# Kernel optimization log

Measured on AMD Instinct MI355X. Metric: run time of the kernel, lower is better.

Reference implementation:

```python
import jax, jax.numpy as jnp
import numpy as np

B, N, DIM = 8, 4096, 512
H, DH = 8, 64
INNER = H * DH
MIN_FREQ = 1.0 / 64
SCALE = 1.0
ROT_DIM = DH // 2  # 32, per spatial axis
EPS = 1e-5


def setup_inputs() -> dict:
    key = jax.random.key(0)
    ks = jax.random.split(key, 6)
    x = jax.random.normal(ks[0], (B, N, DIM), dtype=jnp.float32)
    pos = jax.random.uniform(ks[1], (B, N, 2), dtype=jnp.float32)
    W_qkv = jax.random.normal(ks[2], (3 * INNER, DIM), dtype=jnp.float32) * (1.0 / DH)
    gamma_k = jnp.ones((DH,), jnp.float32)
    beta_k = jnp.zeros((DH,), jnp.float32)
    gamma_v = jnp.ones((DH,), jnp.float32)
    beta_v = jnp.zeros((DH,), jnp.float32)
    W_out = jax.random.normal(ks[3], (DIM, INNER), dtype=jnp.float32) * (1.0 / np.sqrt(INNER))
    b_out = jnp.zeros((DIM,), jnp.float32)
    return {"x": x, "pos": pos, "W_qkv": W_qkv, "gamma_k": gamma_k, "beta_k": beta_k,
            "gamma_v": gamma_v, "beta_v": beta_v, "W_out": W_out, "b_out": b_out}


def _layernorm(t, gamma, beta):
    mu = jnp.mean(t, axis=-1, keepdims=True)
    var = jnp.var(t, axis=-1, keepdims=True)
    return (t - mu) * jax.lax.rsqrt(var + EPS) * gamma + beta


def _rotate_half(t):
    # '... (j d) -> ... j d' with j=2, then cat(-x2, x1)
    d = t.shape[-1] // 2
    x1, x2 = t[..., :d], t[..., d:]
    return jnp.concatenate((-x2, x1), axis=-1)


def _apply_rot(t, freqs):
    return t * jnp.cos(freqs) + _rotate_half(t) * jnp.sin(freqs)


def _freqs(coord):
    # coord: [b, n]; inv_freq over rotary half-dim
    inv_freq = 1.0 / (10000.0 ** (jnp.arange(0, ROT_DIM, 2, dtype=jnp.float32) / ROT_DIM))
    t = coord * (SCALE / MIN_FREQ)
    f = t[..., None] * inv_freq  # [b, n, ROT_DIM//2]
    return jnp.concatenate((f, f), axis=-1)[:, None, :, :]  # [b, 1, n, ROT_DIM]


def reference(x, pos, W_qkv, gamma_k, beta_k, gamma_v, beta_v, W_out, b_out):
    b, n, _ = x.shape
    qkv = x @ W_qkv.T  # [b, n, 3*INNER]
    q, k, v = jnp.split(qkv, 3, axis=-1)
    split = lambda t: t.reshape(b, n, H, DH).transpose(0, 2, 1, 3)  # b h n d
    q, k, v = split(q), split(k), split(v)

    # Galerkin: LayerNorm on K and V over head dim
    k = _layernorm(k, gamma_k, beta_k)
    v = _layernorm(v, gamma_v, beta_v)

    # 2D rotary on q, k: first half of head dim uses x-coords, second half y-coords
    fx, fy = _freqs(pos[..., 0]), _freqs(pos[..., 1])
    rot2d = lambda t: jnp.concatenate(
        (_apply_rot(t[..., :ROT_DIM], fx), _apply_rot(t[..., ROT_DIM:], fy)), axis=-1)
    q = rot2d(q)
    k = rot2d(k)

    # Associative linear attention: (K^T V) then Q @ (.) / n
    dots = jnp.einsum('bhnd,bhne->bhde', k, v)  # [b, h, d, d]
    out = jnp.einsum('bhnd,bhde->bhne', q, dots) * (1.0 / n)
    out = out.transpose(0, 2, 1, 3).reshape(b, n, INNER)
    return out @ W_out.T + b_out
```

## Files before the change

kernel.cpp:

```cpp
#include <hip/hip_runtime.h>
#include <math.h>

#define NB 8
#define NN 4096
#define NDIM 512
#define NH 8
#define NDH 64
#define QKVC 1536
#define NROWS (NB * NN)
#define EPSF 1e-5f
#define INV_N (1.0f / 4096.0f)
#define L2_10K_16 0.8304820237218406f

typedef __bf16 bf16x8_t __attribute__((ext_vector_type(8)));
typedef float f32x4_t __attribute__((ext_vector_type(4)));
typedef unsigned short u16x8 __attribute__((ext_vector_type(8)));

__device__ inline unsigned short f2bf(float f) {
    unsigned u = __builtin_bit_cast(unsigned, f);
    u += 0x7fff + ((u >> 16) & 1);
    return (unsigned short)(u >> 16);
}
__device__ inline float bf2f(unsigned short u) {
    unsigned v = (unsigned)u << 16;
    return __builtin_bit_cast(float, v);
}

#define GLOAD_LDS16(g, s) __builtin_amdgcn_global_load_lds(                    \
    (const __attribute__((address_space(1))) void*)(g),                        \
    (__attribute__((address_space(3))) void*)(s), 16, 0, 0)

#define VMCNT3 asm volatile("s_waitcnt vmcnt(3)" ::: "memory")
#define VMCNT0 asm volatile("s_waitcnt vmcnt(0)" ::: "memory")
#define BARF   { __builtin_amdgcn_s_barrier(); asm volatile("" ::: "memory"); }

__device__ inline void cvt8v(const float* __restrict__ s,
                             unsigned short* __restrict__ d, int i)
{
    float4 a = *(const float4*)(s + i);
    float4 b = *(const float4*)(s + i + 4);
    ushort4 lo, hi;
    lo.x = f2bf(a.x); lo.y = f2bf(a.y); lo.z = f2bf(a.z); lo.w = f2bf(a.w);
    hi.x = f2bf(b.x); hi.y = f2bf(b.y); hi.z = f2bf(b.z); hi.w = f2bf(b.w);
    *(ushort4*)(d + i)     = lo;
    *(ushort4*)(d + i + 4) = hi;
}

__global__ __launch_bounds__(256)
void cvt_all(const float* __restrict__ x,  const float* __restrict__ wq,
             const float* __restrict__ wo,
             unsigned short* __restrict__ xb, unsigned short* __restrict__ wqb,
             unsigned short* __restrict__ wob, float* __restrict__ dots)
{
    const int bid = blockIdx.x, t = threadIdx.x;
    if (bid < 8192) {
        cvt8v(x, xb, (bid * 256 + t) * 8);
    } else if (bid < 8576) {
        cvt8v(wq, wqb, ((bid - 8192) * 256 + t) * 8);
    } else if (bid < 8704) {
        cvt8v(wo, wob, ((bid - 8576) * 256 + t) * 8);
    } else {
        const float4 z = {0.f, 0.f, 0.f, 0.f};
        float4* dp = (float4*)dots + (size_t)((bid - 8704) * 256 + t) * 4;
        dp[0] = z; dp[1] = z; dp[2] = z; dp[3] = z;
    }
}

__global__ __launch_bounds__(512, 4)
void gemm_kv_fused(const unsigned short* __restrict__ A,
                   const unsigned short* __restrict__ Bm,
                   const float* __restrict__ pos,
                   const float* __restrict__ gk, const float* __restrict__ bk,
                   const float* __restrict__ gv, const float* __restrict__ bvv,
                   unsigned short* __restrict__ kT,
                   unsigned short* __restrict__ vT)
{
    __shared__ __align__(16) unsigned short lds[24576];

    const int tid  = threadIdx.x;
    const int wave = tid >> 6;
    const int lane = tid & 63;

    int flat = blockIdx.y * 8 + blockIdx.x;
    flat = (flat & 7) * 128 + (flat >> 3);
    const int bx = flat & 7;
    const int by = flat >> 3;
    const int m0 = by * 256;
    const int n0 = bx * 128;

    const int warp_m = wave >> 1;
    const int warp_n = wave & 1;
    const int fr = lane & 15;
    const int fq = lane >> 4;
    const int ch0 = ((fq ^ ((fr >> 1) & 3)) << 3);

    const int rl = tid >> 2;
    const int cs = (((tid & 3) ^ ((rl >> 1) & 3)) << 3);
    const unsigned short* Asrc = A  + (size_t)(m0 + rl) * NDIM + cs;
    const unsigned short* Bsrc = Bm + (size_t)(n0 + rl) * NDIM + cs;
    const int sdst = wave * 512;

#define STG_A(tt, c) GLOAD_LDS16(Asrc + (size_t)((c) * 128) * NDIM + (tt) * 32, \
        &lds[(((tt) & 1) * 8192) + ((c) * 4096) + sdst])
#define STG_B(tt)    GLOAD_LDS16(Bsrc + (tt) * 32, \
        &lds[16384 + (((tt) & 1) * 4096) + sdst])

    f32x4_t acc[4][4] = {};

    STG_A(0, 0); STG_A(0, 1); STG_B(0);

    #pragma unroll 2
    for (int tt = 0; tt < 16; ++tt) {
        BARF;
        if (tt < 15) { STG_A(tt + 1, 0); STG_A(tt + 1, 1); STG_B(tt + 1); VMCNT3; }
        else VMCNT0;
        BARF;
        bf16x8_t af[4], bfr[4];
        const int ab = (tt & 1) * 8192;
        const int bb = 16384 + (tt & 1) * 4096;
        #pragma unroll
        for (int mi = 0; mi < 4; ++mi)
            af[mi] = *(const bf16x8_t*)&lds[ab + (warp_m * 64 + mi * 16 + fr) * 32 + ch0];
        #pragma unroll
        for (int nj = 0; nj < 4; ++nj)
            bfr[nj] = *(const bf16x8_t*)&lds[bb + (warp_n * 64 + nj * 16 + fr) * 32 + ch0];
        __builtin_amdgcn_s_setprio(1);
        #pragma unroll
        for (int mi = 0; mi < 4; ++mi)
            #pragma unroll
            for (int nj = 0; nj < 4; ++nj)
                acc[mi][nj] = __builtin_amdgcn_mfma_f32_16x16x32_bf16(
                    af[mi], bfr[nj], acc[mi][nj], 0, 0, 0);
        __builtin_amdgcn_s_setprio(0);
    }
#undef STG_A
#undef STG_B

    const int nc = n0 + warp_n * 64;
    const int isK = (nc < 512);
    const int c  = lane & 15;
    const int g4 = (lane >> 4) * 4;
    const int mrow0 = m0 + warp_m * 64;
    const int h = (nc >> 6) & 7;

    {
        const float* gamma = isK ? gk : gv;
        const float* beta  = isK ? bk : bvv;
        float gm[4], bt[4];
        #pragma unroll
        for (int j = 0; j < 4; ++j) { gm[j] = gamma[j * 16 + c]; bt[j] = beta[j * 16 + c]; }
        #pragma unroll
        for (int i = 0; i < 4; ++i)
            #pragma unroll
            for (int r = 0; r < 4; ++r) {
                float t0 = acc[i][0][r], t1 = acc[i][1][r];
                float t2 = acc[i][2][r], t3 = acc[i][3][r];
                float s  = t0 + t1 + t2 + t3;
                float ss = t0*t0 + t1*t1 + t2*t2 + t3*t3;
                #pragma unroll
                for (int msk = 1; msk < 16; msk <<= 1) {
                    s  += __shfl_xor(s,  msk, 64);
                    ss += __shfl_xor(ss, msk, 64);
                }
                const float mu = s * (1.0f / 64.0f);
                const float rs = rsqrtf(ss * (1.0f / 64.0f) - mu * mu + EPSF);
                acc[i][0][r] = (t0 - mu) * rs * gm[0] + bt[0];
                acc[i][1][r] = (t1 - mu) * rs * gm[1] + bt[1];
                acc[i][2][r] = (t2 - mu) * rs * gm[2] + bt[2];
                acc[i][3][r] = (t3 - mu) * rs * gm[3] + bt[3];
            }
    }
    if (isK) {
        const float Kc = 64.0f * exp2f(-(float)c * L2_10K_16);
        #pragma unroll
        for (int i = 0; i < 4; ++i)
            #pragma unroll
            for (int r = 0; r < 4; ++r) {
                const int row = mrow0 + i * 16 + g4 + r;
                const float2 p = ((const float2*)pos)[row];
                float sx, cx, sy, cy;
                __sincosf(p.x * Kc, &sx, &cx);
                __sincosf(p.y * Kc, &sy, &cy);
                const float t0 = acc[i][0][r], t1 = acc[i][1][r];
                const float t2 = acc[i][2][r], t3 = acc[i][3][r];
                acc[i][0][r] = t0 * cx - t1 * sx;
                acc[i][1][r] = t1 * cx + t0 * sx;
                acc[i][2][r] = t2 * cy - t3 * sy;
                acc[i][3][r] = t3 * cy + t2 * sy;
            }
    }
    unsigned short* T = isK ? kT : vT;
    #pragma unroll
    for (int i = 0; i < 4; ++i) {
        const int row = mrow0 + i * 16 + g4;
        const int bb = row >> 12;
        const int nl = row & 4095;
        #pragma unroll
        for (int j = 0; j < 4; ++j) {
            ushort4 o;
            o.x = f2bf(acc[i][j][0]); o.y = f2bf(acc[i][j][1]);
            o.z = f2bf(acc[i][j][2]); o.w = f2bf(acc[i][j][3]);
            *(ushort4*)(T + ((size_t)((bb * NH + h) * 64 + j * 16 + c)) * NN + nl) = o;
        }
    }
}

__global__ __launch_bounds__(512, 4)
void gemm_q_fused(const unsigned short* __restrict__ A,
                  const unsigned short* __restrict__ Bm,
                  const float* __restrict__ pos,
                  unsigned short* __restrict__ qb)
{
    __shared__ __align__(16) unsigned short lds[24576];

    const int tid  = threadIdx.x;
    const int wave = tid >> 6;
    const int lane = tid & 63;

    int flat = blockIdx.y * 4 + blockIdx.x;
    flat = (flat & 7) * 64 + (flat >> 3);
    const int bx = flat & 3;
    const int by = flat >> 2;
    const int m0 = by * 256;
    const int n0 = bx * 128;

    const int warp_m = wave >> 1;
    const int warp_n = wave & 1;
    const int fr = lane & 15;
    const int fq = lane >> 4;
    const int ch0 = ((fq ^ ((fr >> 1) & 3)) << 3);

    const int rl = tid >> 2;
    const int cs = (((tid & 3) ^ ((rl >> 1) & 3)) << 3);
    const unsigned short* Asrc = A  + (size_t)(m0 + rl) * NDIM + cs;
    const unsigned short* Bsrc = Bm + (size_t)(n0 + rl) * NDIM + cs;
    const int sdst = wave * 512;

#define STG_A(tt, c) GLOAD_LDS16(Asrc + (size_t)((c) * 128) * NDIM + (tt) * 32, \
        &lds[(((tt) & 1) * 8192) + ((c) * 4096) + sdst])
#define STG_B(tt)    GLOAD_LDS16(Bsrc + (tt) * 32, \
        &lds[16384 + (((tt) & 1) * 4096) + sdst])

    f32x4_t acc[4][4] = {};

    STG_A(0, 0); STG_A(0, 1); STG_B(0);

    #pragma unroll 2
    for (int tt = 0; tt < 16; ++tt) {
        BARF;
        if (tt < 15) { STG_A(tt + 1, 0); STG_A(tt + 1, 1); STG_B(tt + 1); VMCNT3; }
        else VMCNT0;
        BARF;
        bf16x8_t af[4], bfr[4];
        const int ab = (tt & 1) * 8192;
        const int bb = 16384 + (tt & 1) * 4096;
        #pragma unroll
        for (int mi = 0; mi < 4; ++mi)
            af[mi] = *(const bf16x8_t*)&lds[ab + (warp_m * 64 + mi * 16 + fr) * 32 + ch0];
        #pragma unroll
        for (int nj = 0; nj < 4; ++nj)
            bfr[nj] = *(const bf16x8_t*)&lds[bb + (warp_n * 64 + nj * 16 + fr) * 32 + ch0];
        __builtin_amdgcn_s_setprio(1);
        #pragma unroll
        for (int mi = 0; mi < 4; ++mi)
            #pragma unroll
            for (int nj = 0; nj < 4; ++nj)
                acc[mi][nj] = __builtin_amdgcn_mfma_f32_16x16x32_bf16(
                    af[mi], bfr[nj], acc[mi][nj], 0, 0, 0);
        __builtin_amdgcn_s_setprio(0);
    }
#undef STG_A
#undef STG_B

    const int nc = n0 + warp_n * 64;
    const int c  = lane & 15;
    const int g4 = (lane >> 4) * 4;
    const int mrow0 = m0 + warp_m * 64;

    {
        const float Kc = 64.0f * exp2f(-(float)c * L2_10K_16);
        #pragma unroll
        for (int i = 0; i < 4; ++i)
            #pragma unroll
            for (int r = 0; r < 4; ++r) {
                const int row = mrow0 + i * 16 + g4 + r;
                const float2 p = ((const float2*)pos)[row];
                float sx, cx, sy, cy;
                __sincosf(p.x * Kc, &sx, &cx);
                __sincosf(p.y * Kc, &sy, &cy);
                const float t0 = acc[i][0][r], t1 = acc[i][1][r];
                const float t2 = acc[i][2][r], t3 = acc[i][3][r];
                acc[i][0][r] = t0 * cx - t1 * sx;
                acc[i][1][r] = t1 * cx + t0 * sx;
                acc[i][2][r] = t2 * cy - t3 * sy;
                acc[i][3][r] = t3 * cy + t2 * sy;
            }
    }
    #pragma unroll
    for (int i = 0; i < 4; ++i)
        #pragma unroll
        for (int j = 0; j < 4; ++j) {
            unsigned short* qp = qb + (size_t)(mrow0 + i * 16 + g4) * NDIM
                               + nc + j * 16 + c;
            #pragma unroll
            for (int r = 0; r < 4; ++r)
                qp[(size_t)r * NDIM] = f2bf(acc[i][j][r]);
        }
}

__global__ __launch_bounds__(256)
void dots_mfma(const unsigned short* __restrict__ kT,
               const unsigned short* __restrict__ vT,
               float* __restrict__ dots)
{
    __shared__ __align__(16) unsigned short sk[2][64 * 64];
    __shared__ __align__(16) unsigned short sv[2][64 * 64];
    const int t = threadIdx.x;
    const int w = t >> 6, l = t & 63;
    const int bh = blockIdx.z * NH + blockIdx.y;
    const int n0 = blockIdx.x * 512;

    const int r8 = l >> 3;
    const int cs = ((l & 7) ^ r8) * 8;
    const unsigned short* ksrc = kT + (size_t)(bh * 64 + w * 16 + r8) * NN + n0 + cs;
    const unsigned short* vsrc = vT + (size_t)(bh * 64 + w * 16 + r8) * NN + n0 + cs;

#define STGK(buf, kt, q) GLOAD_LDS16(ksrc + (size_t)(q) * 8 * NN + (kt), \
        &sk[buf][w * 1024 + (q) * 512])
#define STGV(buf, kt, q) GLOAD_LDS16(vsrc + (size_t)(q) * 8 * NN + (kt), \
        &sv[buf][w * 1024 + (q) * 512])

    const int fr = l & 15, fq = l >> 4;
    const int doff = (w >> 1) * 32, eoff = (w & 1) * 32;

    f32x4_t acc[2][2] = {};

    STGK(0, 0, 0); STGK(0, 0, 1); STGV(0, 0, 0); STGV(0, 0, 1);

    for (int s = 0; s < 8; ++s) {
        const int buf = s & 1;
        asm volatile("s_waitcnt vmcnt(0)" ::: "memory");
        __builtin_amdgcn_s_barrier();
        bf16x8_t ak[2][2], bv[2][2];
        #pragma unroll
        for (int di = 0; di < 2; ++di)
            #pragma unroll
            for (int ks = 0; ks < 2; ++ks)
                ak[di][ks] = *(const bf16x8_t*)
                    &sk[buf][(doff + di * 16 + fr) * 64 + (((ks * 4 + fq) ^ (fr & 7)) * 8)];
        #pragma unroll
        for (int ej = 0; ej < 2; ++ej)
            #pragma unroll
            for (int ks = 0; ks < 2; ++ks)
                bv[ej][ks] = *(const bf16x8_t*)
                    &sv[buf][(eoff + ej * 16 + fr) * 64 + (((ks * 4 + fq) ^ (fr & 7)) * 8)];
        if (s + 1 < 8) {
            const int nb = buf ^ 1, kt = (s + 1) * 64;
            STGK(nb, kt, 0); STGK(nb, kt, 1); STGV(nb, kt, 0); STGV(nb, kt, 1);
        }
        #pragma unroll
        for (int ks = 0; ks < 2; ++ks)
            #pragma unroll
            for (int di = 0; di < 2; ++di)
                #pragma unroll
                for (int ej = 0; ej < 2; ++ej)
                    acc[di][ej] = __builtin_amdgcn_mfma_f32_16x16x32_bf16(
                        ak[di][ks], bv[ej][ks], acc[di][ej], 0, 0, 0);
    }
#undef STGK
#undef STGV

    float* dp = dots + (size_t)bh * 64 * 64;
    const int cc = l & 15;
    const int rr = (l >> 4) * 4;
    #pragma unroll
    for (int di = 0; di < 2; ++di)
        #pragma unroll
        for (int ej = 0; ej < 2; ++ej)
            #pragma unroll
            for (int r = 0; r < 4; ++r)
                atomicAdd(dp + (doff + di * 16 + rr + r) * 64 + eoff + ej * 16 + cc,
                          acc[di][ej][r]);
}

__global__ __launch_bounds__(256)
void dotsw_mfma(const unsigned short* __restrict__ Woutb,
                const float* __restrict__ dots,
                unsigned short* __restrict__ M2b)
{
    __shared__ unsigned short As[128 * 64];
    __shared__ unsigned short Bs[64 * 64];
    const int t = threadIdx.x;
    const int wave = t >> 6;
    const int lane = t & 63;
    const int dp0 = blockIdx.x * 128;
    const int h = blockIdx.y, b = blockIdx.z;

    const int srow = lane >> 3;
    const int scol = (lane & 7) * 8;
    const unsigned short* Ag = Woutb + (size_t)(dp0 + wave * 32 + srow) * NDIM
                             + h * NDH + scol;
    #pragma unroll
    for (int i = 0; i < 4; ++i)
        GLOAD_LDS16(Ag + (size_t)i * 8 * NDIM, As + wave * 2048 + i * 512);

    {
        const float* Dg = dots + (size_t)(b * NH + h) * 4096;
        const int dr = t >> 2;
        const int dc = (t & 3) * 16;
        const float* dgp = Dg + dr * 64 + dc;
        float4 f0 = *(const float4*)(dgp);
        float4 f1 = *(const float4*)(dgp + 4);
        float4 f2 = *(const float4*)(dgp + 8);
        float4 f3 = *(const float4*)(dgp + 12);
        ushort4 o0, o1, o2, o3;
        o0.x = f2bf(f0.x * INV_N); o0.y = f2bf(f0.y * INV_N);
        o0.z = f2bf(f0.z * INV_N); o0.w = f2bf(f0.w * INV_N);
        o1.x = f2bf(f1.x * INV_N); o1.y = f2bf(f1.y * INV_N);
        o1.z = f2bf(f1.z * INV_N); o1.w = f2bf(f1.w * INV_N);
        o2.x = f2bf(f2.x * INV_N); o2.y = f2bf(f2.y * INV_N);
        o2.z = f2bf(f2.z * INV_N); o2.w = f2bf(f2.w * INV_N);
        o3.x = f2bf(f3.x * INV_N); o3.y = f2bf(f3.y * INV_N);
        o3.z = f2bf(f3.z * INV_N); o3.w = f2bf(f3.w * INV_N);
        *(ushort4*)&Bs[dr * 64 + dc]      = o0;
        *(ushort4*)&Bs[dr * 64 + dc + 4]  = o1;
        *(ushort4*)&Bs[dr * 64 + dc + 8]  = o2;
        *(ushort4*)&Bs[dr * 64 + dc + 12] = o3;
    }
    __syncthreads();

    const int wm = (wave >> 1) * 64;
    const int wn = (wave & 1) * 32;
    const int fr = lane & 15;
    const int fq = (lane >> 4) * 8;

    f32x4_t acc[4][2] = {};
    #pragma unroll
    for (int kk = 0; kk < 2; ++kk) {
        bf16x8_t af[4], bf[2];
        #pragma unroll
        for (int i = 0; i < 4; ++i)
            af[i] = *(const bf16x8_t*)&As[(wm + i * 16 + fr) * 64 + kk * 32 + fq];
        #pragma unroll
        for (int j = 0; j < 2; ++j)
            bf[j] = *(const bf16x8_t*)&Bs[(wn + j * 16 + fr) * 64 + kk * 32 + fq];
        #pragma unroll
        for (int i = 0; i < 4; ++i)
            #pragma unroll
            for (int j = 0; j < 2; ++j)
                acc[i][j] = __builtin_amdgcn_mfma_f32_16x16x32_bf16(
                    af[i], bf[j], acc[i][j], 0, 0, 0);
    }

    const int c  = lane & 15;
    const int g4 = (lane >> 4) * 4;
    #pragma unroll
    for (int i = 0; i < 4; ++i)
        #pragma unroll
        for (int j = 0; j < 2; ++j) {
            unsigned short* mp = M2b + ((size_t)(b * NDIM) + dp0 + wm + i * 16 + g4) * NDIM
                               + h * NDH + wn + j * 16 + c;
            #pragma unroll
            for (int r = 0; r < 4; ++r)
                mp[(size_t)r * NDIM] = f2bf(acc[i][j][r]);
        }
}

__global__ __launch_bounds__(512, 4)
void gemm_out_mfma(const unsigned short* __restrict__ qb,
                   const unsigned short* __restrict__ M2b,
                   const float* __restrict__ bias, float* __restrict__ C)
{
    __shared__ __align__(16) unsigned short lds[24576];

    const int tid  = threadIdx.x;
    const int wave = tid >> 6;
    const int lane = tid & 63;

    int flat = blockIdx.y * 4 + blockIdx.x;
    flat = (flat & 7) * 64 + (flat >> 3);
    const int bx = flat & 3;
    const int by = flat >> 2;
    const int m0 = by * 256;
    const int n0 = bx * 128;
    const int b  = m0 >> 12;

    const int warp_m = wave >> 1;
    const int warp_n = wave & 1;
    const int fr = lane & 15;
    const int fq = lane >> 4;
    const int ch0 = ((fq ^ ((fr >> 1) & 3)) << 3);

    const int rl = tid >> 2;
    const int cs = (((tid & 3) ^ ((rl >> 1) & 3)) << 3);
    const unsigned short* Asrc = qb + (size_t)(m0 + rl) * NDIM + cs;
    const unsigned short* Bsrc = M2b + (size_t)b * NDIM * NDIM
                               + (size_t)(n0 + rl) * NDIM + cs;
    const int sdst = wave * 512;

#define STG_A(tt, c) GLOAD_LDS16(Asrc + (size_t)((c) * 128) * NDIM + (tt) * 32, \
        &lds[(((tt) & 1) * 8192) + ((c) * 4096) + sdst])
#define STG_B(tt)    GLOAD_LDS16(Bsrc + (tt) * 32, \
        &lds[16384 + (((tt) & 1) * 4096) + sdst])

    f32x4_t acc[4][4] = {};

    STG_A(0, 0); STG_A(0, 1); STG_B(0);

    #pragma unroll 2
    for (int tt = 0; tt < 16; ++tt) {
        BARF;
        if (tt < 15) { STG_A(tt + 1, 0); STG_A(tt + 1, 1); STG_B(tt + 1); VMCNT3; }
        else VMCNT0;
        BARF;
        bf16x8_t af[4], bfr[4];
        const int ab = (tt & 1) * 8192;
        const int bb = 16384 + (tt & 1) * 4096;
        #pragma unroll
        for (int mi = 0; mi < 4; ++mi)
            af[mi] = *(const bf16x8_t*)&lds[ab + (warp_m * 64 + mi * 16 + fr) * 32 + ch0];
        #pragma unroll
        for (int nj = 0; nj < 4; ++nj)
            bfr[nj] = *(const bf16x8_t*)&lds[bb + (warp_n * 64 + nj * 16 + fr) * 32 + ch0];
        __builtin_amdgcn_s_setprio(1);
        #pragma unroll
        for (int mi = 0; mi < 4; ++mi)
            #pragma unroll
            for (int nj = 0; nj < 4; ++nj)
                acc[mi][nj] = __builtin_amdgcn_mfma_f32_16x16x32_bf16(
                    af[mi], bfr[nj], acc[mi][nj], 0, 0, 0);
        __builtin_amdgcn_s_setprio(0);
    }
#undef STG_A
#undef STG_B

    const int c  = lane & 15;
    const int g4 = (lane >> 4) * 4;
    const int mrow0 = m0 + warp_m * 64;
    const int ncol = n0 + warp_n * 64;

    #pragma unroll
    for (int j = 0; j < 4; ++j) {
        const int col = ncol + j * 16 + c;
        const float bb = bias[col];
        #pragma unroll
        for (int i = 0; i < 4; ++i) {
            float* cp = C + (size_t)(mrow0 + i * 16 + g4) * NDIM + col;
            #pragma unroll
            for (int r = 0; r < 4; ++r)
                cp[(size_t)r * NDIM] = acc[i][j][r] + bb;
        }
    }
}

extern "C" void kernel_launch(void* const* d_in, const int* in_sizes, int n_in,
                              void* d_out, int out_size, void* d_ws, size_t ws_size,
                              hipStream_t stream)
{
    const float* x    = (const float*)d_in[0];
    const float* pos  = (const float*)d_in[1];
    const float* Wqkv = (const float*)d_in[2];
    const float* gk   = (const float*)d_in[3];
    const float* bk   = (const float*)d_in[4];
    const float* gv   = (const float*)d_in[5];
    const float* bv   = (const float*)d_in[6];
    const float* Wout = (const float*)d_in[7];
    const float* bout = (const float*)d_in[8];
    float* out = (float*)d_out;

    float* dots = (float*)d_ws;
    unsigned short* M2b     = (unsigned short*)(dots + (size_t)NB * NH * 64 * 64);
    unsigned short* qb      = M2b + (size_t)NB * NDIM * NDIM;
    unsigned short* kT      = qb + (size_t)NROWS * NDIM;
    unsigned short* vT      = kT + (size_t)NB * NH * NDH * NN;
    unsigned short* xb      = vT + (size_t)NB * NH * NDH * NN;
    unsigned short* Wqkvb   = xb + (size_t)NROWS * NDIM;
    unsigned short* Woutb   = Wqkvb + (size_t)QKVC * NDIM;

    cvt_all<<<dim3(8768), dim3(256), 0, stream>>>(x, Wqkv, Wout, xb, Wqkvb, Woutb, dots);
    gemm_kv_fused<<<dim3(8, NROWS / 256), dim3(512), 0, stream>>>(
        xb, Wqkvb + (size_t)512 * NDIM, pos, gk, bk, gv, bv, kT, vT);
    gemm_q_fused<<<dim3(4, NROWS / 256), dim3(512), 0, stream>>>(
        xb, Wqkvb, pos, qb);
    dots_mfma<<<dim3(NN / 512, NH, NB), dim3(256), 0, stream>>>(kT, vT, dots);
    dotsw_mfma<<<dim3(NDIM / 128, NH, NB), dim3(256), 0, stream>>>(Woutb, dots, M2b);
    gemm_out_mfma<<<dim3(NDIM / 128, NROWS / 256), dim3(512), 0, stream>>>(
        qb, M2b, bout, out);
}
```

Measured before the change: 265.1 us.

## Triple-buffer LDS staging in GEMMs and dots kernel with one barrier per step

Replaces the double-buffered LDS pipeline in the three GEMM kernels (now sharing a GEMM_CORE macro) with a three-stage ring that prefetches two tiles ahead. This lets each iteration use a single barrier instead of two. The dots kernel gets the same three-stage, two-ahead prefetch with a partial vmcnt wait and raised MFMA priority. The cost is 50% more LDS per block (72KB for the GEMMs), which could reduce how many blocks fit on a CU.

```diff
diff --git a/kernel.cpp b/kernel.cpp
--- a/kernel.cpp
+++ b/kernel.cpp
@@ -30,6 +30,7 @@
     (const __attribute__((address_space(1))) void*)(g),                        \
     (__attribute__((address_space(3))) void*)(s), 16, 0, 0)
 
+#define VMCNT4 asm volatile("s_waitcnt vmcnt(4)" ::: "memory")
 #define VMCNT3 asm volatile("s_waitcnt vmcnt(3)" ::: "memory")
 #define VMCNT0 asm volatile("s_waitcnt vmcnt(0)" ::: "memory")
 #define BARF   { __builtin_amdgcn_s_barrier(); asm volatile("" ::: "memory"); }
@@ -66,6 +67,47 @@
     }
 }
 
+#define GEMM_CORE(Asrc_, Bsrc_)                                                \
+    f32x4_t acc[4][4] = {};                                                    \
+    const int fr = lane & 15;                                                  \
+    const int fq = lane >> 4;                                                  \
+    const int ch0 = ((fq ^ ((fr >> 1) & 3)) << 3);                             \
+    const int rl = tid >> 2;                                                   \
+    const int cs = (((tid & 3) ^ ((rl >> 1) & 3)) << 3);                       \
+    const unsigned short* Asrc = (Asrc_) + (size_t)rl * NDIM + cs;             \
+    const unsigned short* Bsrc = (Bsrc_) + (size_t)rl * NDIM + cs;             \
+    const int sdst = wave * 512;                                               \
+    STG_A(0, 0); STG_A(0, 1); STG_B(0);                                        \
+    STG_A(1, 0); STG_A(1, 1); STG_B(1);                                        \
+    _Pragma("unroll")                                                          \
+    for (int tt = 0; tt < 16; ++tt) {                                          \
+        if (tt == 15) VMCNT0; else VMCNT3;                                     \
+        BARF;                                                                  \
+        if (tt < 14) { STG_A(tt + 2, 0); STG_A(tt + 2, 1); STG_B(tt + 2); }    \
+        bf16x8_t af[4], bfr[4];                                                \
+        const int ab = (tt % 3) * 12288;                                       \
+        const int bb = ab + 8192;                                              \
+        _Pragma("unroll")                                                      \
+        for (int mi = 0; mi < 4; ++mi)                                         \
+            af[mi] = *(const bf16x8_t*)&lds[ab + (warp_m * 64 + mi * 16 + fr) * 32 + ch0]; \
+        _Pragma("unroll")                                                      \
+        for (int nj = 0; nj < 4; ++nj)                                         \
+            bfr[nj] = *(const bf16x8_t*)&lds[bb + (warp_n * 64 + nj * 16 + fr) * 32 + ch0]; \
+        __builtin_amdgcn_s_setprio(1);                                         \
+        _Pragma("unroll")                                                      \
+        for (int mi = 0; mi < 4; ++mi)                                         \
+            _Pragma("unroll")                                                  \
+            for (int nj = 0; nj < 4; ++nj)                                     \
+                acc[mi][nj] = __builtin_amdgcn_mfma_f32_16x16x32_bf16(         \
+                    af[mi], bfr[nj], acc[mi][nj], 0, 0, 0);                    \
+        __builtin_amdgcn_s_setprio(0);                                         \
+    }
+
+#define STG_A(tt, c) GLOAD_LDS16(Asrc + (size_t)((c) * 128) * NDIM + (tt) * 32, \
+        &lds[((tt) % 3) * 12288 + ((c) * 4096) + sdst])
+#define STG_B(tt)    GLOAD_LDS16(Bsrc + (tt) * 32, \
+        &lds[((tt) % 3) * 12288 + 8192 + sdst])
+
 __global__ __launch_bounds__(512, 4)
 void gemm_kv_fused(const unsigned short* __restrict__ A,
                    const unsigned short* __restrict__ Bm,
@@ -75,7 +117,7 @@
                    unsigned short* __restrict__ kT,
                    unsigned short* __restrict__ vT)
 {
-    __shared__ __align__(16) unsigned short lds[24576];
+    __shared__ __align__(16) unsigned short lds[36864];
 
     const int tid  = threadIdx.x;
     const int wave = tid >> 6;
@@ -90,51 +132,8 @@
 
     const int warp_m = wave >> 1;
     const int warp_n = wave & 1;
-    const int fr = lane & 15;
-    const int fq = lane >> 4;
-    const int ch0 = ((fq ^ ((fr >> 1) & 3)) << 3);
-
-    const int rl = tid >> 2;
-    const int cs = (((tid & 3) ^ ((rl >> 1) & 3)) << 3);
-    const unsigned short* Asrc = A  + (size_t)(m0 + rl) * NDIM + cs;
-    const unsigned short* Bsrc = Bm + (size_t)(n0 + rl) * NDIM + cs;
-    const int sdst = wave * 512;
-
-#define STG_A(tt, c) GLOAD_LDS16(Asrc + (size_t)((c) * 128) * NDIM + (tt) * 32, \
-        &lds[(((tt) & 1) * 8192) + ((c) * 4096) + sdst])
-#define STG_B(tt)    GLOAD_LDS16(Bsrc + (tt) * 32, \
-        &lds[16384 + (((tt) & 1) * 4096) + sdst])
-
-    f32x4_t acc[4][4] = {};
-
-    STG_A(0, 0); STG_A(0, 1); STG_B(0);
-
-    #pragma unroll 2
-    for (int tt = 0; tt < 16; ++tt) {
-        BARF;
-        if (tt < 15) { STG_A(tt + 1, 0); STG_A(tt + 1, 1); STG_B(tt + 1); VMCNT3; }
-        else VMCNT0;
-        BARF;
-        bf16x8_t af[4], bfr[4];
-        const int ab = (tt & 1) * 8192;
-        const int bb = 16384 + (tt & 1) * 4096;
-        #pragma unroll
-        for (int mi = 0; mi < 4; ++mi)
-            af[mi] = *(const bf16x8_t*)&lds[ab + (warp_m * 64 + mi * 16 + fr) * 32 + ch0];
-        #pragma unroll
-        for (int nj = 0; nj < 4; ++nj)
-            bfr[nj] = *(const bf16x8_t*)&lds[bb + (warp_n * 64 + nj * 16 + fr) * 32 + ch0];
-        __builtin_amdgcn_s_setprio(1);
-        #pragma unroll
-        for (int mi = 0; mi < 4; ++mi)
-            #pragma unroll
-            for (int nj = 0; nj < 4; ++nj)
-                acc[mi][nj] = __builtin_amdgcn_mfma_f32_16x16x32_bf16(
-                    af[mi], bfr[nj], acc[mi][nj], 0, 0, 0);
-        __builtin_amdgcn_s_setprio(0);
-    }
-#undef STG_A
-#undef STG_B
+
+    GEMM_CORE(A + (size_t)m0 * NDIM, Bm + (size_t)n0 * NDIM)
 
     const int nc = n0 + warp_n * 64;
     const int isK = (nc < 512);
@@ -193,14 +192,14 @@
     #pragma unroll
     for (int i = 0; i < 4; ++i) {
         const int row = mrow0 + i * 16 + g4;
-        const int bb = row >> 12;
+        const int bb2 = row >> 12;
         const int nl = row & 4095;
         #pragma unroll
         for (int j = 0; j < 4; ++j) {
             ushort4 o;
             o.x = f2bf(acc[i][j][0]); o.y = f2bf(acc[i][j][1]);
             o.z = f2bf(acc[i][j][2]); o.w = f2bf(acc[i][j][3]);
-            *(ushort4*)(T + ((size_t)((bb * NH + h) * 64 + j * 16 + c)) * NN + nl) = o;
+            *(ushort4*)(T + ((size_t)((bb2 * NH + h) * 64 + j * 16 + c)) * NN + nl) = o;
         }
     }
 }
@@ -211,7 +210,7 @@
                   const float* __restrict__ pos,
                   unsigned short* __restrict__ qb)
 {
-    __shared__ __align__(16) unsigned short lds[24576];
+    __shared__ __align__(16) unsigned short lds[36864];
 
     const int tid  = threadIdx.x;
     const int wave = tid >> 6;
@@ -226,51 +225,8 @@
 
     const int warp_m = wave >> 1;
     const int warp_n = wave & 1;
-    const int fr = lane & 15;
-    const int fq = lane >> 4;
-    const int ch0 = ((fq ^ ((fr >> 1) & 3)) << 3);
-
-    const int rl = tid >> 2;
-    const int cs = (((tid & 3) ^ ((rl >> 1) & 3)) << 3);
-    const unsigned short* Asrc = A  + (size_t)(m0 + rl) * NDIM + cs;
-    const unsigned short* Bsrc = Bm + (size_t)(n0 + rl) * NDIM + cs;
-    const int sdst = wave * 512;
-
-#define STG_A(tt, c) GLOAD_LDS16(Asrc + (size_t)((c) * 128) * NDIM + (tt) * 32, \
-        &lds[(((tt) & 1) * 8192) + ((c) * 4096) + sdst])
-#define STG_B(tt)    GLOAD_LDS16(Bsrc + (tt) * 32, \
-        &lds[16384 + (((tt) & 1) * 4096) + sdst])
-
-    f32x4_t acc[4][4] = {};
-
-    STG_A(0, 0); STG_A(0, 1); STG_B(0);
-
-    #pragma unroll 2
-    for (int tt = 0; tt < 16; ++tt) {
-        BARF;
-        if (tt < 15) { STG_A(tt + 1, 0); STG_A(tt + 1, 1); STG_B(tt + 1); VMCNT3; }
-        else VMCNT0;
-        BARF;
-        bf16x8_t af[4], bfr[4];
-        const int ab = (tt & 1) * 8192;
-        const int bb = 16384 + (tt & 1) * 4096;
-        #pragma unroll
-        for (int mi = 0; mi < 4; ++mi)
-            af[mi] = *(const bf16x8_t*)&lds[ab + (warp_m * 64 + mi * 16 + fr) * 32 + ch0];
-        #pragma unroll
-        for (int nj = 0; nj < 4; ++nj)
-            bfr[nj] = *(const bf16x8_t*)&lds[bb + (warp_n * 64 + nj * 16 + fr) * 32 + ch0];
-        __builtin_amdgcn_s_setprio(1);
-        #pragma unroll
-        for (int mi = 0; mi < 4; ++mi)
-            #pragma unroll
-            for (int nj = 0; nj < 4; ++nj)
-                acc[mi][nj] = __builtin_amdgcn_mfma_f32_16x16x32_bf16(
-                    af[mi], bfr[nj], acc[mi][nj], 0, 0, 0);
-        __builtin_amdgcn_s_setprio(0);
-    }
-#undef STG_A
-#undef STG_B
+
+    GEMM_CORE(A + (size_t)m0 * NDIM, Bm + (size_t)n0 * NDIM)
 
     const int nc = n0 + warp_n * 64;
     const int c  = lane & 15;
@@ -308,13 +264,57 @@
         }
 }
 
+__global__ __launch_bounds__(512, 4)
+void gemm_out_mfma(const unsigned short* __restrict__ qb,
+                   const unsigned short* __restrict__ M2b,
+                   const float* __restrict__ bias, float* __restrict__ C)
+{
+    __shared__ __align__(16) unsigned short lds[36864];
+
+    const int tid  = threadIdx.x;
+    const int wave = tid >> 6;
+    const int lane = tid & 63;
+
+    int flat = blockIdx.y * 4 + blockIdx.x;
+    flat = (flat & 7) * 64 + (flat >> 3);
+    const int bx = flat & 3;
+    const int by = flat >> 2;
+    const int m0 = by * 256;
+    const int n0 = bx * 128;
+    const int b  = m0 >> 12;
+
+    const int warp_m = wave >> 1;
+    const int warp_n = wave & 1;
+
+    GEMM_CORE(qb + (size_t)m0 * NDIM,
+              M2b + (size_t)b * NDIM * NDIM + (size_t)n0 * NDIM)
+
+    const int c  = lane & 15;
+    const int g4 = (lane >> 4) * 4;
+    const int mrow0 = m0 + warp_m * 64;
+    const int ncol = n0 + warp_n * 64;
+
+    #pragma unroll
+    for (int j = 0; j < 4; ++j) {
+        const int col = ncol + j * 16 + c;
+        const float bb2 = bias[col];
+        #pragma unroll
+        for (int i = 0; i < 4; ++i) {
+            float* cp = C + (size_t)(mrow0 + i * 16 + g4) * NDIM + col;
+            #pragma unroll
+            for (int r = 0; r < 4; ++r)
+                cp[(size_t)r * NDIM] = acc[i][j][r] + bb2;
+        }
+    }
+}
+
 __global__ __launch_bounds__(256)
 void dots_mfma(const unsigned short* __restrict__ kT,
                const unsigned short* __restrict__ vT,
                float* __restrict__ dots)
 {
-    __shared__ __align__(16) unsigned short sk[2][64 * 64];
-    __shared__ __align__(16) unsigned short sv[2][64 * 64];
+    __shared__ __align__(16) unsigned short sk[3][64 * 64];
+    __shared__ __align__(16) unsigned short sv[3][64 * 64];
     const int t = threadIdx.x;
     const int w = t >> 6, l = t & 63;
     const int bh = blockIdx.z * NH + blockIdx.y;
@@ -325,22 +325,26 @@
     const unsigned short* ksrc = kT + (size_t)(bh * 64 + w * 16 + r8) * NN + n0 + cs;
     const unsigned short* vsrc = vT + (size_t)(bh * 64 + w * 16 + r8) * NN + n0 + cs;
 
-#define STGK(buf, kt, q) GLOAD_LDS16(ksrc + (size_t)(q) * 8 * NN + (kt), \
-        &sk[buf][w * 1024 + (q) * 512])
-#define STGV(buf, kt, q) GLOAD_LDS16(vsrc + (size_t)(q) * 8 * NN + (kt), \
-        &sv[buf][w * 1024 + (q) * 512])
+#define STGK(ss, q) GLOAD_LDS16(ksrc + (size_t)(q) * 8 * NN + (ss) * 64, \
+        &sk[(ss) % 3][w * 1024 + (q) * 512])
+#define STGV(ss, q) GLOAD_LDS16(vsrc + (size_t)(q) * 8 * NN + (ss) * 64, \
+        &sv[(ss) % 3][w * 1024 + (q) * 512])
 
     const int fr = l & 15, fq = l >> 4;
     const int doff = (w >> 1) * 32, eoff = (w & 1) * 32;
 
     f32x4_t acc[2][2] = {};
 
-    STGK(0, 0, 0); STGK(0, 0, 1); STGV(0, 0, 0); STGV(0, 0, 1);
-
+    STGK(0, 0); STGK(0, 1); STGV(0, 0); STGV(0, 1);
+    STGK(1, 0); STGK(1, 1); STGV(1, 0); STGV(1, 1);
+
+    #pragma unroll
     for (int s = 0; s < 8; ++s) {
-        const int buf = s & 1;
-        asm volatile("s_waitcnt vmcnt(0)" ::: "memory");
+        if (s == 7) VMCNT0; else VMCNT4;
         __builtin_amdgcn_s_barrier();
+        asm volatile("" ::: "memory");
+        if (s < 6) { STGK(s + 2, 0); STGK(s + 2, 1); STGV(s + 2, 0); STGV(s + 2, 1); }
+        const int buf = s % 3;
         bf16x8_t ak[2][2], bv[2][2];
         #pragma unroll
         for (int di = 0; di < 2; ++di)
@@ -354,10 +358,7 @@
             for (int ks = 0; ks < 2; ++ks)
                 bv[ej][ks] = *(const bf16x8_t*)
                     &sv[buf][(eoff + ej * 16 + fr) * 64 + (((ks * 4 + fq) ^ (fr & 7)) * 8)];
-        if (s + 1 < 8) {
-            const int nb = buf ^ 1, kt = (s + 1) * 64;
-            STGK(nb, kt, 0); STGK(nb, kt, 1); STGV(nb, kt, 0); STGV(nb, kt, 1);
-        }
+        __builtin_amdgcn_s_setprio(1);
         #pragma unroll
         for (int ks = 0; ks < 2; ++ks)
             #pragma unroll
@@ -366,6 +367,7 @@
                 for (int ej = 0; ej < 2; ++ej)
                     acc[di][ej] = __builtin_amdgcn_mfma_f32_16x16x32_bf16(
                         ak[di][ks], bv[ej][ks], acc[di][ej], 0, 0, 0);
+        __builtin_amdgcn_s_setprio(0);
     }
 #undef STGK
 #undef STGV
@@ -466,93 +468,6 @@
         }
 }
 
-__global__ __launch_bounds__(512, 4)
-void gemm_out_mfma(const unsigned short* __restrict__ qb,
-                   const unsigned short* __restrict__ M2b,
-                   const float* __restrict__ bias, float* __restrict__ C)
-{
-    __shared__ __align__(16) unsigned short lds[24576];
-
-    const int tid  = threadIdx.x;
-    const int wave = tid >> 6;
-    const int lane = tid & 63;
-
-    int flat = blockIdx.y * 4 + blockIdx.x;
-    flat = (flat & 7) * 64 + (flat >> 3);
-    const int bx = flat & 3;
-    const int by = flat >> 2;
-    const int m0 = by * 256;
-    const int n0 = bx * 128;
-    const int b  = m0 >> 12;
-
-    const int warp_m = wave >> 1;
-    const int warp_n = wave & 1;
-    const int fr = lane & 15;
-    const int fq = lane >> 4;
-    const int ch0 = ((fq ^ ((fr >> 1) & 3)) << 3);
-
-    const int rl = tid >> 2;
-    const int cs = (((tid & 3) ^ ((rl >> 1) & 3)) << 3);
-    const unsigned short* Asrc = qb + (size_t)(m0 + rl) * NDIM + cs;
-    const unsigned short* Bsrc = M2b + (size_t)b * NDIM * NDIM
-                               + (size_t)(n0 + rl) * NDIM + cs;
-    const int sdst = wave * 512;
-
-#define STG_A(tt, c) GLOAD_LDS16(Asrc + (size_t)((c) * 128) * NDIM + (tt) * 32, \
-        &lds[(((tt) & 1) * 8192) + ((c) * 4096) + sdst])
-#define STG_B(tt)    GLOAD_LDS16(Bsrc + (tt) * 32, \
-        &lds[16384 + (((tt) & 1) * 4096) + sdst])
-
-    f32x4_t acc[4][4] = {};
-
-    STG_A(0, 0); STG_A(0, 1); STG_B(0);
-
-    #pragma unroll 2
-    for (int tt = 0; tt < 16; ++tt) {
-        BARF;
-        if (tt < 15) { STG_A(tt + 1, 0); STG_A(tt + 1, 1); STG_B(tt + 1); VMCNT3; }
-        else VMCNT0;
-        BARF;
-        bf16x8_t af[4], bfr[4];
-        const int ab = (tt & 1) * 8192;
-        const int bb = 16384 + (tt & 1) * 4096;
-        #pragma unroll
-        for (int mi = 0; mi < 4; ++mi)
-            af[mi] = *(const bf16x8_t*)&lds[ab + (warp_m * 64 + mi * 16 + fr) * 32 + ch0];
-        #pragma unroll
-        for (int nj = 0; nj < 4; ++nj)
-            bfr[nj] = *(const bf16x8_t*)&lds[bb + (warp_n * 64 + nj * 16 + fr) * 32 + ch0];
-        __builtin_amdgcn_s_setprio(1);
-        #pragma unroll
-        for (int mi = 0; mi < 4; ++mi)
-            #pragma unroll
-            for (int nj = 0; nj < 4; ++nj)
-                acc[mi][nj] = __builtin_amdgcn_mfma_f32_16x16x32_bf16(
-                    af[mi], bfr[nj], acc[mi][nj], 0, 0, 0);
-        __builtin_amdgcn_s_setprio(0);
-    }
-#undef STG_A
-#undef STG_B
-
-    const int c  = lane & 15;
-    const int g4 = (lane >> 4) * 4;
-    const int mrow0 = m0 + warp_m * 64;
-    const int ncol = n0 + warp_n * 64;
-
-    #pragma unroll
-    for (int j = 0; j < 4; ++j) {
-        const int col = ncol + j * 16 + c;
-        const float bb = bias[col];
-        #pragma unroll
-        for (int i = 0; i < 4; ++i) {
-            float* cp = C + (size_t)(mrow0 + i * 16 + g4) * NDIM + col;
-            #pragma unroll
-            for (int r = 0; r < 4; ++r)
-                cp[(size_t)r * NDIM] = acc[i][j][r] + bb;
-        }
-    }
-}
-
 extern "C" void kernel_launch(void* const* d_in, const int* in_sizes, int n_in,
                               void* d_out, int out_size, void* d_ws, size_t ws_size,
                               hipStream_t stream)
```

New measurement: 271.3 us. 1.02x slower.
